# Performance work log

Measured on AMD Instinct MI355X. Metric: run time of the kernel, lower is better.

Reference implementation:

```python
import jax, jax.numpy as jnp
import numpy as np

DIM = 768
H = 12
NUM_PROP = 40
SPARSITY = 0.05
ALPHA = 0.1
ATTN_KEEP = 0.75  # attention threshold quantile index fraction
EPS = 1e-5


def layernorm(x, w, b):
    mu = x.mean(-1, keepdims=True)
    var = ((x - mu) ** 2).mean(-1, keepdims=True)
    return (x - mu) * jax.lax.rsqrt(var + EPS) * w + b


def setup_inputs() -> dict:
    key = jax.random.key(0)
    ks = jax.random.split(key, 8)
    C, Hd = DIM, DIM
    mlp_h = 4 * DIM
    s = 0.02
    return {
        "x": jax.random.normal(ks[0], (64, 197, C), dtype=jnp.float32),
        "norm1_w": jnp.ones((C,), jnp.float32),
        "norm1_b": jnp.zeros((C,), jnp.float32),
        "qkv_w": jax.random.normal(ks[1], (3 * C, C), jnp.float32) * s,
        "proj_w": jax.random.normal(ks[2], (C, C), jnp.float32) * s,
        "proj_b": jnp.zeros((C,), jnp.float32),
        "norm2_w": jnp.ones((C,), jnp.float32),
        "norm2_b": jnp.zeros((C,), jnp.float32),
        "fc1_w": jax.random.normal(ks[3], (mlp_h, C), jnp.float32) * s,
        "fc1_b": jnp.zeros((mlp_h,), jnp.float32),
        "fc2_w": jax.random.normal(ks[4], (C, mlp_h), jnp.float32) * s,
        "fc2_b": jnp.zeros((C,), jnp.float32),
    }


def _forward(x, norm1_w, norm1_b, qkv_w, proj_w, proj_b,
             norm2_w, norm2_b, fc1_w, fc1_b, fc2_w, fc2_b):
    B, N, C = x.shape
    hd = C // H
    scale = hd ** -0.5

    h = layernorm(x, norm1_w, norm1_b)
    qkv = (h @ qkv_w.T).reshape(B, N, 3, H, hd).transpose(2, 0, 3, 1, 4)
    q, k, v = qkv[0], qkv[1], qkv[2]          # [B,H,N,hd]
    attn = jax.nn.softmax((q * scale) @ k.transpose(0, 1, 3, 2), axis=-1)
    attn_rank = jnp.sort(attn.reshape(B, H, -1), axis=-1)[..., ::-1]
    sigma = attn_rank[:, :, int(N * N * ATTN_KEEP)][:, :, None, None]
    attn = jnp.where(attn >= sigma, attn, 0.0)
    out = (attn @ v).transpose(0, 2, 1, 3).reshape(B, N, C)
    x = x + out @ proj_w.T + proj_b

    # ---- select: DiagAttnMean ----
    diag = jnp.diagonal(attn, axis1=-2, axis2=-1)        # [B,H,N]
    token_rank = diag[:, :, 1:].mean(1)                  # [B,N-1]
    order = jnp.argsort(-token_rank, axis=1)             # descending
    index_kept = order[:, :-NUM_PROP] + 1                # [B, num_kept]
    index_elim = order[:, -NUM_PROP:] + 1                # [B, num_elim]
    num_kept = N - 1 - NUM_PROP
    num_elim = NUM_PROP

    # ---- propagate: ThresholdGraph (multihead, thresholded) ----
    x_kept = jnp.take_along_axis(x, index_kept[:, :, None], axis=1)
    x_elim = jnp.take_along_axis(x, index_elim[:, :, None], axis=1)
    x_cls = x[:, 0:1]
    w = jnp.take_along_axis(attn, index_kept[:, None, :, None], axis=2)  # [B,H,k,N]
    w = jnp.take_along_axis(w, index_elim[:, None, None, :], axis=3)     # [B,H,k,e]
    w_rank = jnp.sort(w.reshape(B, H, -1), axis=-1)[..., ::-1]
    w_sigma = w_rank[:, :, int(num_elim * num_kept * SPARSITY)][:, :, None, None]
    w = jnp.where(w >= w_sigma, w, 0.0)
    xe = x_elim.reshape(B, num_elim, H, hd)
    x_prop = jnp.einsum('bhke,behd->bkhd', w, xe).reshape(B, num_kept, C)
    x_kept = x_kept + ALPHA * x_prop
    x = jnp.concatenate((x_cls, x_kept), axis=1)         # [B, N-num_prop, C]

    # ---- MLP ----
    h = layernorm(x, norm2_w, norm2_b)
    h = jax.nn.gelu(h @ fc1_w.T + fc1_b, approximate=False)
    x = x + h @ fc2_w.T + fc2_b
    return x


def reference(x, norm1_w, norm1_b, qkv_w, proj_w, proj_b,
              norm2_w, norm2_b, fc1_w, fc1_b, fc2_w, fc2_b):
    return _forward(x, norm1_w, norm1_b, qkv_w, proj_w, proj_b,
                    norm2_w, norm2_b, fc1_w, fc1_b, fc2_w, fc2_b)
```

## Files before the change

### kernel.cpp

```cpp
#include <hip/hip_runtime.h>
#include <math.h>

constexpr int B_  = 64;
constexpr int N_  = 197;
constexpr int C_  = 768;
constexpr int H_  = 12;
constexpr int HD_ = 64;
constexpr int NP_ = 40;
constexpr int NK_ = 156;
constexpr int N1_ = 196;
constexpr int N2_ = 157;
constexpr int MLP_ = 3072;
constexpr int M1_ = B_ * N_;
constexpr int M2_ = B_ * N2_;
constexpr int M1P_ = 12672;
constexpr int M2P_ = 10112;
constexpr float SCALE_ = 0.125f;
constexpr float ALPHA_ = 0.1f;
constexpr float EPS_   = 1e-5f;
constexpr int KASC_ATTN = N_ * N_ - 1 - 29106;
constexpr int KASC_W    = NK_ * NP_ - 1 - 312;

typedef __bf16 bf16x8 __attribute__((ext_vector_type(8)));
typedef float  floatx4 __attribute__((ext_vector_type(4)));

constexpr size_t A_B     = 0;
constexpr size_t OFFB_XAHI = A_B;
constexpr size_t OFFB_XALO = A_B + 19464192;
constexpr size_t OFFB_ATTN = A_B;
constexpr size_t OFFB_FC1H = A_B;
constexpr size_t OFFB_H2   = A_B + 62128128;
constexpr size_t OFFB_FC1W = A_B + 77660160;
constexpr size_t OFFB_FC2W = A_B + 82378752;
constexpr size_t B_B     = 119221248;
constexpr size_t OFFB_QHI  = B_B;
constexpr size_t OFFB_QLO  = B_B + 38928384;
constexpr size_t OFFB_VB   = B_B + 77856768;
constexpr size_t OFFB_X1   = B_B;
constexpr size_t OFFB_AOUT = B_B + 38928384;
constexpr size_t OFFB_WBUF = B_B + 77856768;
constexpr size_t W_B     = 216542208;
constexpr size_t OFFB_QWHI = W_B;
constexpr size_t OFFB_QWLO = W_B + 3538944;
constexpr size_t OFFB_PRJW = W_B + 7077888;
constexpr size_t S_B     = 224799744;
constexpr size_t OFFB_SIG  = S_B;
constexpr size_t OFFB_WSIG = S_B + 3072;
constexpr size_t OFFB_TR   = S_B + 6144;
constexpr size_t OFFB_ORD  = S_B + 56320;

__global__ __launch_bounds__(256) void wsplit_kernel(
    const float* __restrict__ w, __bf16* __restrict__ hi,
    __bf16* __restrict__ lo, int n)
{
  const int i = blockIdx.x * 256 + threadIdx.x;
  if (i >= n) return;
  const float v = w[i];
  const __bf16 h = (__bf16)v;
  hi[i] = h;
  lo[i] = (__bf16)(v - (float)h);
}

__global__ __launch_bounds__(256) void wconv_kernel(
    const float* __restrict__ w, __bf16* __restrict__ o, int n)
{
  const int i = blockIdx.x * 256 + threadIdx.x;
  if (i < n) o[i] = (__bf16)w[i];
}

__device__ __forceinline__ float block_reduce_sum(float v, float* red) {
  #pragma unroll
  for (int off = 32; off; off >>= 1) v += __shfl_xor(v, off);
  if ((threadIdx.x & 63) == 0) red[threadIdx.x >> 6] = v;
  __syncthreads();
  float r = red[0] + red[1] + red[2] + red[3];
  __syncthreads();
  return r;
}

__global__ __launch_bounds__(256) void ln_bf16_kernel(
    const float* __restrict__ x, const float* __restrict__ w,
    const float* __restrict__ b, __bf16* __restrict__ ohi,
    __bf16* __restrict__ olo, int Mvalid)
{
  __shared__ float red[4];
  const size_t row = blockIdx.x;
  const int t = threadIdx.x;
  if ((int)row >= Mvalid) {
    #pragma unroll
    for (int i = 0; i < 3; ++i) {
      ohi[row * C_ + t + 256 * i] = (__bf16)0.f;
      if (olo) olo[row * C_ + t + 256 * i] = (__bf16)0.f;
    }
    return;
  }
  const float* xr = x + row * C_;
  float v[3];
  float s = 0.f;
  #pragma unroll
  for (int i = 0; i < 3; ++i) { v[i] = xr[t + 256 * i]; s += v[i]; }
  const float mu = block_reduce_sum(s, red) * (1.f / 768.f);
  s = 0.f;
  #pragma unroll
  for (int i = 0; i < 3; ++i) { float d = v[i] - mu; s += d * d; }
  const float var = block_reduce_sum(s, red) * (1.f / 768.f);
  const float rs = rsqrtf(var + EPS_);
  #pragma unroll
  for (int i = 0; i < 3; ++i) {
    const int c = t + 256 * i;
    const float val = (v[i] - mu) * rs * w[c] + b[c];
    const __bf16 h = (__bf16)val;
    ohi[row * C_ + c] = h;
    if (olo) olo[row * C_ + c] = (__bf16)(val - (float)h);
  }
}

__device__ __forceinline__ void stage_tile(
    const __bf16* __restrict__ gbase, int ldg, __bf16* lds, int wave, int lane)
{
  #pragma unroll
  for (int j = 0; j < 2; ++j) {
    const int seg = 4 * j + wave;
    const int row = seg * 16 + (lane >> 2);
    const int col = (lane & 3) * 8;
    const __bf16* g = gbase + (size_t)row * ldg + col;
    __bf16* l = lds + seg * 512 + lane * 8;
    __builtin_amdgcn_global_load_lds(
        (const __attribute__((address_space(1))) unsigned int*)g,
        (__attribute__((address_space(3))) unsigned int*)l, 16, 0, 0);
  }
}

__device__ __forceinline__ bf16x8 frag(const __bf16* lds, int r, int hi8) {
  return *(const bf16x8*)(lds + r * 32 + hi8);
}

__global__ __launch_bounds__(256) void gemm_bf16_kernel(
    const __bf16* __restrict__ A, const __bf16* __restrict__ Bw,
    const float* __restrict__ bias, const float* __restrict__ res,
    float* __restrict__ outf, __bf16* __restrict__ outb,
    int Mstore, int Nn, int K, int act)
{
  __shared__ __bf16 As[128 * 32];
  __shared__ __bf16 Bs[128 * 32];
  const int t = threadIdx.x;
  const int wave = t >> 6, lane = t & 63;
  const int m0 = blockIdx.y * 128, n0 = blockIdx.x * 128;
  const int wm = (wave >> 1) * 64, wn = (wave & 1) * 64;
  const int lo = lane & 15, hi8 = (lane >> 4) * 8;
  floatx4 acc[4][4] = {};
  for (int k0 = 0; k0 < K; k0 += 32) {
    stage_tile(A + (size_t)m0 * K + k0, K, As, wave, lane);
    stage_tile(Bw + (size_t)n0 * K + k0, K, Bs, wave, lane);
    __syncthreads();
    bf16x8 af[4], bfr[4];
    #pragma unroll
    for (int i = 0; i < 4; ++i) af[i]  = frag(As, wm + i * 16 + lo, hi8);
    #pragma unroll
    for (int j = 0; j < 4; ++j) bfr[j] = frag(Bs, wn + j * 16 + lo, hi8);
    #pragma unroll
    for (int i = 0; i < 4; ++i)
      #pragma unroll
      for (int j = 0; j < 4; ++j)
        acc[i][j] = __builtin_amdgcn_mfma_f32_16x16x32_bf16(
            af[i], bfr[j], acc[i][j], 0, 0, 0);
    __syncthreads();
  }
  #pragma unroll
  for (int i = 0; i < 4; ++i) {
    #pragma unroll
    for (int j = 0; j < 4; ++j) {
      #pragma unroll
      for (int r = 0; r < 4; ++r) {
        const int m = m0 + wm + i * 16 + (lane >> 4) * 4 + r;
        const int n = n0 + wn + j * 16 + lo;
        if (m < Mstore) {
          float v = acc[i][j][r];
          if (bias) v += bias[n];
          if (act) v = 0.5f * v * (1.0f + erff(v * 0.7071067811865476f));
          if (res) v += res[(size_t)m * Nn + n];
          if (outf) outf[(size_t)m * Nn + n] = v;
          else      outb[(size_t)m * Nn + n] = (__bf16)v;
        }
      }
    }
  }
}

__global__ __launch_bounds__(256) void gemm_split_kernel(
    const __bf16* __restrict__ Ah, const __bf16* __restrict__ Al,
    const __bf16* __restrict__ Bh, const __bf16* __restrict__ Bl,
    __bf16* __restrict__ outhi, __bf16* __restrict__ outlo, int Nn, int K)
{
  __shared__ __bf16 Ahs[128 * 32];
  __shared__ __bf16 Als[128 * 32];
  __shared__ __bf16 Bhs[128 * 32];
  __shared__ __bf16 Bls[128 * 32];
  const int t = threadIdx.x;
  const int wave = t >> 6, lane = t & 63;
  const int m0 = blockIdx.y * 128, n0 = blockIdx.x * 128;
  const int wm = (wave >> 1) * 64, wn = (wave & 1) * 64;
  const int lo = lane & 15, hi8 = (lane >> 4) * 8;
  floatx4 acc[4][4] = {};
  for (int k0 = 0; k0 < K; k0 += 32) {
    stage_tile(Ah + (size_t)m0 * K + k0, K, Ahs, wave, lane);
    stage_tile(Al + (size_t)m0 * K + k0, K, Als, wave, lane);
    stage_tile(Bh + (size_t)n0 * K + k0, K, Bhs, wave, lane);
    stage_tile(Bl + (size_t)n0 * K + k0, K, Bls, wave, lane);
    __syncthreads();
    bf16x8 ah[4], al[4], bh[4], bl[4];
    #pragma unroll
    for (int i = 0; i < 4; ++i) {
      ah[i] = frag(Ahs, wm + i * 16 + lo, hi8);
      al[i] = frag(Als, wm + i * 16 + lo, hi8);
    }
    #pragma unroll
    for (int j = 0; j < 4; ++j) {
      bh[j] = frag(Bhs, wn + j * 16 + lo, hi8);
      bl[j] = frag(Bls, wn + j * 16 + lo, hi8);
    }
    #pragma unroll
    for (int i = 0; i < 4; ++i)
      #pragma unroll
      for (int j = 0; j < 4; ++j) {
        acc[i][j] = __builtin_amdgcn_mfma_f32_16x16x32_bf16(
            ah[i], bh[j], acc[i][j], 0, 0, 0);
        acc[i][j] = __builtin_amdgcn_mfma_f32_16x16x32_bf16(
            ah[i], bl[j], acc[i][j], 0, 0, 0);
        acc[i][j] = __builtin_amdgcn_mfma_f32_16x16x32_bf16(
            al[i], bh[j], acc[i][j], 0, 0, 0);
      }
    __syncthreads();
  }
  #pragma unroll
  for (int i = 0; i < 4; ++i)
    #pragma unroll
    for (int j = 0; j < 4; ++j)
      #pragma unroll
      for (int r = 0; r < 4; ++r) {
        const int m = m0 + wm + i * 16 + (lane >> 4) * 4 + r;
        const int n = n0 + wn + j * 16 + lo;
        const float v = acc[i][j][r];
        const __bf16 h = (__bf16)v;
        outhi[(size_t)m * Nn + n] = h;
        outlo[(size_t)m * Nn + n] = (__bf16)(v - (float)h);
      }
}

__global__ __launch_bounds__(256) void scores_mfma_kernel(
    const __bf16* __restrict__ qhi, const __bf16* __restrict__ qlo,
    float* __restrict__ attn)
{
  const int bh = blockIdx.x;
  const int b = bh / H_, h = bh % H_;
  __shared__ __bf16 Khi[208 * 72];
  __shared__ __bf16 Klo[208 * 72];
  const int t = threadIdx.x;
  for (int idx = t; idx < 208 * 32; idx += 256) {
    const int j = idx >> 5;
    const int c2 = (idx & 31) * 2;
    unsigned int vh = 0u, vl = 0u;
    if (j < N_) {
      const size_t g = ((size_t)(b * N_ + j)) * 1536 + 768 + h * HD_ + c2;
      vh = *(const unsigned int*)(qhi + g);
      vl = *(const unsigned int*)(qlo + g);
    }
    *(unsigned int*)(Khi + j * 72 + c2) = vh;
    *(unsigned int*)(Klo + j * 72 + c2) = vl;
  }
  __syncthreads();
  const int wave = t >> 6, lane = t & 63;
  const int lo16 = lane & 15, k8 = (lane >> 4) * 8;
  float* Sbh = attn + (size_t)bh * N_ * N_;
  bf16x8 zf;
  #pragma unroll
  for (int e = 0; e < 8; ++e) zf[e] = (__bf16)0.f;
  for (int i = 0; i < 4; ++i) {
    const int mrow = wave * 64 + i * 16 + lo16;
    bf16x8 ahi[2], alo[2];
    #pragma unroll
    for (int kk = 0; kk < 2; ++kk) {
      if (mrow < N_) {
        const size_t g = ((size_t)(b * N_ + mrow)) * 1536 + h * HD_ + kk * 32 + k8;
        ahi[kk] = *(const bf16x8*)(qhi + g);
        alo[kk] = *(const bf16x8*)(qlo + g);
      } else {
        ahi[kk] = zf;
        alo[kk] = zf;
      }
    }
    for (int j = 0; j < 13; ++j) {
      floatx4 acc = {0.f, 0.f, 0.f, 0.f};
      #pragma unroll
      for (int kk = 0; kk < 2; ++kk) {
        const bf16x8 bh_ = *(const bf16x8*)(Khi + (j * 16 + lo16) * 72 + kk * 32 + k8);
        const bf16x8 bl_ = *(const bf16x8*)(Klo + (j * 16 + lo16) * 72 + kk * 32 + k8);
        acc = __builtin_amdgcn_mfma_f32_16x16x32_bf16(ahi[kk], bh_, acc, 0, 0, 0);
        acc = __builtin_amdgcn_mfma_f32_16x16x32_bf16(ahi[kk], bl_, acc, 0, 0, 0);
        acc = __builtin_amdgcn_mfma_f32_16x16x32_bf16(alo[kk], bh_, acc, 0, 0, 0);
        acc = __builtin_amdgcn_mfma_f32_16x16x32_bf16(alo[kk], bl_, acc, 0, 0, 0);
      }
      const int col = j * 16 + lo16;
      if (col < N_) {
        #pragma unroll
        for (int r = 0; r < 4; ++r) {
          const int row = wave * 64 + i * 16 + (lane >> 4) * 4 + r;
          if (row < N_) Sbh[(size_t)row * N_ + col] = acc[r] * SCALE_;
        }
      }
    }
  }
}

__global__ __launch_bounds__(256) void softmax_kernel(float* __restrict__ attn)
{
  const int row = blockIdx.x * 4 + (threadIdx.x >> 6);
  const int lane = threadIdx.x & 63;
  float* r = attn + (size_t)row * N_;
  float vals[4];
  float m = -1e30f;
  int cnt = 0;
  for (int j = lane; j < N_; j += 64) { vals[cnt] = r[j]; m = fmaxf(m, vals[cnt]); ++cnt; }
  #pragma unroll
  for (int off = 32; off; off >>= 1) m = fmaxf(m, __shfl_xor(m, off));
  float s = 0.f;
  for (int i = 0; i < cnt; ++i) { vals[i] = expf(vals[i] - m); s += vals[i]; }
  #pragma unroll
  for (int off = 32; off; off >>= 1) s += __shfl_xor(s, off);
  const float inv = 1.0f / s;
  cnt = 0;
  for (int j = lane; j < N_; j += 64) { r[j] = vals[cnt] * inv; ++cnt; }
}

__global__ __launch_bounds__(256) void radix_select_kernel(
    const float* __restrict__ data, int count, int k, int stride,
    float* __restrict__ out)
{
  const float* seg = data + (size_t)blockIdx.x * stride;
  __shared__ unsigned int hist[256];
  __shared__ unsigned int prefix_s;
  __shared__ int k_s;
  unsigned int prefix = 0u;
  int kk = k;
  for (int pass = 3; pass >= 0; --pass) {
    const int shift = pass * 8;
    hist[threadIdx.x] = 0u;
    __syncthreads();
    const unsigned int mask_known =
        (pass == 3) ? 0u : (0xFFFFFFFFu << ((pass + 1) * 8));
    for (int i = threadIdx.x; i < count; i += 256) {
      const unsigned int bits = __float_as_uint(seg[i]);
      if ((bits & mask_known) == prefix)
        atomicAdd(&hist[(bits >> shift) & 0xFFu], 1u);
    }
    __syncthreads();
    if (threadIdx.x == 0) {
      int rem = kk;
      unsigned int d = 0;
      for (; d < 256u; ++d) {
        if (rem < (int)hist[d]) break;
        rem -= (int)hist[d];
      }
      prefix_s = prefix | (d << shift);
      k_s = rem;
    }
    __syncthreads();
    prefix = prefix_s;
    kk = k_s;
    __syncthreads();
  }
  if (threadIdx.x == 0) out[blockIdx.x] = __uint_as_float(prefix);
}

__global__ __launch_bounds__(256) void threshold_kernel(
    float* __restrict__ a, const float* __restrict__ sig, int total, int seglen)
{
  const int idx = blockIdx.x * 256 + threadIdx.x;
  if (idx >= total) return;
  const float v = a[idx];
  if (v < sig[idx / seglen]) a[idx] = 0.0f;
}

__global__ __launch_bounds__(256) void attn_v_mfma_kernel(
    const float* __restrict__ attn, const float* __restrict__ sig,
    const __bf16* __restrict__ v, __bf16* __restrict__ out)
{
  const int bh = blockIdx.x;
  const int mt = blockIdx.y;
  const int b = bh / H_, h = bh % H_;
  __shared__ __bf16 Ps[64 * 232];
  __shared__ __bf16 Vt[64 * 232];
  const int t = threadIdx.x;
  const float sigbh = sig[bh];
  const float* abase = attn + (size_t)bh * N_ * N_;
  for (int idx = t; idx < 64 * 112; idx += 256) {
    const int r = idx / 112;
    const int j0 = (idx % 112) * 2;
    const int gr = mt * 64 + r;
    float v0 = 0.f, v1 = 0.f;
    if (gr < N_) {
      if (j0 < N_)     { const float a0 = abase[(size_t)gr * N_ + j0];     v0 = (a0 >= sigbh) ? a0 : 0.f; }
      if (j0 + 1 < N_) { const float a1 = abase[(size_t)gr * N_ + j0 + 1]; v1 = (a1 >= sigbh) ? a1 : 0.f; }
    }
    __bf16 p2[2] = {(__bf16)v0, (__bf16)v1};
    *(unsigned int*)(Ps + r * 232 + j0) = *(unsigned int*)p2;
  }
  for (int idx = t; idx < 64 * 224; idx += 256) {
    const int d = idx / 224;
    const int j = idx % 224;
    __bf16 val = (__bf16)0.f;
    if (j < N_) val = v[((size_t)(b * N_ + j)) * C_ + h * HD_ + d];
    Vt[d * 232 + j] = val;
  }
  __syncthreads();
  const int wave = t >> 6, lane = t & 63;
  const int lo16 = lane & 15, k8 = (lane >> 4) * 8;
  #pragma unroll
  for (int jn = 0; jn < 4; ++jn) {
    floatx4 acc = {0.f, 0.f, 0.f, 0.f};
    #pragma unroll
    for (int kk = 0; kk < 7; ++kk) {
      const bf16x8 a = *(const bf16x8*)(Ps + (wave * 16 + lo16) * 232 + kk * 32 + k8);
      const bf16x8 bb = *(const bf16x8*)(Vt + (jn * 16 + lo16) * 232 + kk * 32 + k8);
      acc = __builtin_amdgcn_mfma_f32_16x16x32_bf16(a, bb, acc, 0, 0, 0);
    }
    const int d = jn * 16 + lo16;
    #pragma unroll
    for (int r = 0; r < 4; ++r) {
      const int m = mt * 64 + wave * 16 + (lane >> 4) * 4 + r;
      if (m < N_)
        out[((size_t)b * N_ + m) * C_ + h * HD_ + d] = (__bf16)acc[r];
    }
  }
}

__global__ __launch_bounds__(256) void token_rank_kernel(
    const float* __restrict__ attn, const float* __restrict__ sig,
    float* __restrict__ tr)
{
  const int b = blockIdx.x;
  for (int j = threadIdx.x; j < N1_; j += 256) {
    const int n = j + 1;
    float s = 0.f;
    #pragma unroll
    for (int h = 0; h < H_; ++h) {
      const float d = attn[(((size_t)(b * H_ + h)) * N_ + n) * N_ + n];
      s += (d >= sig[b * H_ + h]) ? d : 0.f;
    }
    tr[b * N1_ + j] = s * (1.f / H_);
  }
}

__global__ __launch_bounds__(256) void order_kernel(
    const float* __restrict__ tr, int* __restrict__ order)
{
  const int b = blockIdx.x;
  __shared__ float v[N1_];
  const int t = threadIdx.x;
  if (t < N1_) v[t] = tr[b * N1_ + t];
  __syncthreads();
  if (t < N1_) {
    const float mv = v[t];
    int r = 0;
    for (int i = 0; i < N1_; ++i) {
      const float vi = v[i];
      r += (vi > mv) || (vi == mv && i < t);
    }
    order[b * N1_ + r] = t;
  }
}

__global__ __launch_bounds__(256) void w_gather_kernel(
    const float* __restrict__ attn, const float* __restrict__ sig,
    const int* __restrict__ ord, float* __restrict__ w)
{
  const int idx = blockIdx.x * 256 + threadIdx.x;
  if (idx >= B_ * H_ * NK_ * NP_) return;
  const int e = idx % NP_;
  const int k = (idx / NP_) % NK_;
  const int h = (idx / (NP_ * NK_)) % H_;
  const int b = idx / (NP_ * NK_ * H_);
  const int ki = ord[b * N1_ + k] + 1;
  const int ej = ord[b * N1_ + NK_ + e] + 1;
  const float v = attn[(((size_t)b * H_ + h) * N_ + ki) * N_ + ej];
  w[idx] = (v >= sig[b * H_ + h]) ? v : 0.f;
}

__global__ __launch_bounds__(256) void xprop_kernel(
    const float* __restrict__ x1, const float* __restrict__ w,
    const int* __restrict__ ord, float* __restrict__ x2)
{
  const int b = blockIdx.y;
  const int kk = blockIdx.x;
  const int t = threadIdx.x;
  if (kk == 0) {
    for (int c = t; c < C_; c += 256)
      x2[(size_t)b * N2_ * C_ + c] = x1[(size_t)b * N_ * C_ + c];
    return;
  }
  const int k = kk - 1;
  __shared__ float ws_[H_ * NP_];
  __shared__ int es[NP_];
  if (t < NP_) es[t] = ord[b * N1_ + NK_ + t] + 1;
  for (int i = t; i < H_ * NP_; i += 256) {
    const int h = i / NP_, e = i % NP_;
    ws_[i] = w[(((size_t)b * H_ + h) * NK_ + k) * NP_ + e];
  }
  __syncthreads();
  const int kept = ord[b * N1_ + k] + 1;
  const float* xk = x1 + ((size_t)b * N_ + kept) * C_;
  float* xo = x2 + ((size_t)b * N2_ + 1 + k) * C_;
  for (int c = t; c < C_; c += 256) {
    const int h = c >> 6;
    float acc = 0.f;
    #pragma unroll 8
    for (int e = 0; e < NP_; ++e)
      acc += ws_[h * NP_ + e] * x1[((size_t)b * N_ + es[e]) * C_ + c];
    xo[c] = xk[c] + ALPHA_ * acc;
  }
}

extern "C" void kernel_launch(void* const* d_in, const int* in_sizes, int n_in,
                              void* d_out, int out_size, void* d_ws, size_t ws_size,
                              hipStream_t stream)
{
  const float* x     = (const float*)d_in[0];
  const float* n1w   = (const float*)d_in[1];
  const float* n1b   = (const float*)d_in[2];
  const float* qkvw  = (const float*)d_in[3];
  const float* projw = (const float*)d_in[4];
  const float* projb = (const float*)d_in[5];
  const float* n2w   = (const float*)d_in[6];
  const float* n2b   = (const float*)d_in[7];
  const float* fc1w  = (const float*)d_in[8];
  const float* fc1b  = (const float*)d_in[9];
  const float* fc2w  = (const float*)d_in[10];
  const float* fc2b  = (const float*)d_in[11];
  float* outp = (float*)d_out;

  char* ws = (char*)d_ws;
  __bf16* xa_hi = (__bf16*)(ws + OFFB_XAHI);
  __bf16* xa_lo = (__bf16*)(ws + OFFB_XALO);
  float*  attn  = (float*)(ws + OFFB_ATTN);
  __bf16* fc1h  = (__bf16*)(ws + OFFB_FC1H);
  __bf16* h2    = (__bf16*)(ws + OFFB_H2);
  __bf16* fc1wb = (__bf16*)(ws + OFFB_FC1W);
  __bf16* fc2wb = (__bf16*)(ws + OFFB_FC2W);
  __bf16* qhi   = (__bf16*)(ws + OFFB_QHI);
  __bf16* qlo   = (__bf16*)(ws + OFFB_QLO);
  __bf16* vb    = (__bf16*)(ws + OFFB_VB);
  float*  x1    = (float*)(ws + OFFB_X1);
  __bf16* aout  = (__bf16*)(ws + OFFB_AOUT);
  float*  wbuf  = (float*)(ws + OFFB_WBUF);
  __bf16* qwhi  = (__bf16*)(ws + OFFB_QWHI);
  __bf16* qwlo  = (__bf16*)(ws + OFFB_QWLO);
  __bf16* prjwb = (__bf16*)(ws + OFFB_PRJW);
  float*  sig   = (float*)(ws + OFFB_SIG);
  float*  wsig  = (float*)(ws + OFFB_WSIG);
  float*  tr    = (float*)(ws + OFFB_TR);
  int*    ord   = (int*)(ws + OFFB_ORD);
  float*  x2    = outp;

  wsplit_kernel<<<(2304 * 768 + 255) / 256, 256, 0, stream>>>(
      qkvw, qwhi, qwlo, 2304 * 768);
  wconv_kernel<<<(768 * 768 + 255) / 256, 256, 0, stream>>>(
      projw, prjwb, 768 * 768);
  ln_bf16_kernel<<<M1P_, 256, 0, stream>>>(x, n1w, n1b, xa_hi, xa_lo, M1_);
  gemm_split_kernel<<<dim3(1536 / 128, M1P_ / 128), 256, 0, stream>>>(
      xa_hi, xa_lo, qwhi, qwlo, qhi, qlo, 1536, C_);
  gemm_bf16_kernel<<<dim3(C_ / 128, M1P_ / 128), 256, 0, stream>>>(
      xa_hi, qwhi + (size_t)1536 * C_, nullptr, nullptr, nullptr, vb,
      M1P_, C_, C_, 0);
  scores_mfma_kernel<<<B_ * H_, 256, 0, stream>>>(qhi, qlo, attn);
  softmax_kernel<<<(B_ * H_ * N_) / 4, 256, 0, stream>>>(attn);
  radix_select_kernel<<<B_ * H_, 256, 0, stream>>>(attn, N_ * N_, KASC_ATTN,
                                                   N_ * N_, sig);
  attn_v_mfma_kernel<<<dim3(B_ * H_, 4), 256, 0, stream>>>(attn, sig, vb, aout);
  token_rank_kernel<<<B_, 256, 0, stream>>>(attn, sig, tr);
  order_kernel<<<B_, 256, 0, stream>>>(tr, ord);
  gemm_bf16_kernel<<<dim3(C_ / 128, M1P_ / 128), 256, 0, stream>>>(
      aout, prjwb, projb, x, x1, nullptr, M1_, C_, C_, 0);
  {
    const int total = B_ * H_ * NK_ * NP_;
    w_gather_kernel<<<(total + 255) / 256, 256, 0, stream>>>(attn, sig, ord, wbuf);
    radix_select_kernel<<<B_ * H_, 256, 0, stream>>>(wbuf, NK_ * NP_, KASC_W,
                                                     NK_ * NP_, wsig);
    threshold_kernel<<<(total + 255) / 256, 256, 0, stream>>>(wbuf, wsig, total,
                                                              NK_ * NP_);
  }
  wconv_kernel<<<(MLP_ * C_ + 255) / 256, 256, 0, stream>>>(
      fc1w, fc1wb, MLP_ * C_);
  wconv_kernel<<<(C_ * MLP_ + 255) / 256, 256, 0, stream>>>(
      fc2w, fc2wb, C_ * MLP_);
  xprop_kernel<<<dim3(N2_, B_), 256, 0, stream>>>(x1, wbuf, ord, x2);
  ln_bf16_kernel<<<M2P_, 256, 0, stream>>>(x2, n2w, n2b, h2, nullptr, M2_);
  gemm_bf16_kernel<<<dim3(MLP_ / 128, M2P_ / 128), 256, 0, stream>>>(
      h2, fc1wb, fc1b, nullptr, nullptr, fc1h, M2P_, MLP_, C_, 1);
  gemm_bf16_kernel<<<dim3(C_ / 128, M2P_ / 128), 256, 0, stream>>>(
      fc1h, fc2wb, fc2b, x2, outp, nullptr, M2_, C_, MLP_, 0);
}
```

Baseline: 1.367 ms.

## Split radix select into multi-block histogram passes with wave-aggregated atomics

Replaces the single-block-per-segment radix select with a multi-kernel scheme: each of the four 8-bit passes launches a histogram kernel that spreads each segment across several blocks (8 for attention, 2 for the gathered weights), followed by a small scan kernel that updates the prefix and remaining rank. Shared-memory histogram increments are aggregated per wave with ballot/match to reduce atomic contention on hot bins. The goal is more parallelism, since 768 blocks each serially scanned about 39k elements four times. The cost is many more kernel launches, global atomics, and a serial per-segment scan done by one thread each.

```diff
diff --git a/kernel.cpp b/kernel.cpp
--- a/kernel.cpp
+++ b/kernel.cpp
@@ -20,6 +20,7 @@
 constexpr float EPS_   = 1e-5f;
 constexpr int KASC_ATTN = N_ * N_ - 1 - 29106;
 constexpr int KASC_W    = NK_ * NP_ - 1 - 312;
+constexpr int NSEG_ = B_ * H_;
 
 typedef __bf16 bf16x8 __attribute__((ext_vector_type(8)));
 typedef float  floatx4 __attribute__((ext_vector_type(4)));
@@ -48,6 +49,9 @@
 constexpr size_t OFFB_WSIG = S_B + 3072;
 constexpr size_t OFFB_TR   = S_B + 6144;
 constexpr size_t OFFB_ORD  = S_B + 56320;
+constexpr size_t OFFB_HIST = S_B + 106496;
+constexpr size_t OFFB_PFX  = S_B + 892928;
+constexpr size_t OFFB_KK   = S_B + 896000;
 
 __global__ __launch_bounds__(256) void wsplit_kernel(
     const float* __restrict__ w, __bf16* __restrict__ hi,
@@ -332,44 +336,78 @@
   for (int j = lane; j < N_; j += 64) { r[j] = vals[cnt] * inv; ++cnt; }
 }
 
-__global__ __launch_bounds__(256) void radix_select_kernel(
-    const float* __restrict__ data, int count, int k, int stride,
-    float* __restrict__ out)
-{
-  const float* seg = data + (size_t)blockIdx.x * stride;
-  __shared__ unsigned int hist[256];
-  __shared__ unsigned int prefix_s;
-  __shared__ int k_s;
-  unsigned int prefix = 0u;
-  int kk = k;
-  for (int pass = 3; pass >= 0; --pass) {
-    const int shift = pass * 8;
-    hist[threadIdx.x] = 0u;
-    __syncthreads();
-    const unsigned int mask_known =
-        (pass == 3) ? 0u : (0xFFFFFFFFu << ((pass + 1) * 8));
-    for (int i = threadIdx.x; i < count; i += 256) {
-      const unsigned int bits = __float_as_uint(seg[i]);
-      if ((bits & mask_known) == prefix)
-        atomicAdd(&hist[(bits >> shift) & 0xFFu], 1u);
-    }
-    __syncthreads();
-    if (threadIdx.x == 0) {
-      int rem = kk;
-      unsigned int d = 0;
-      for (; d < 256u; ++d) {
-        if (rem < (int)hist[d]) break;
-        rem -= (int)hist[d];
-      }
-      prefix_s = prefix | (d << shift);
-      k_s = rem;
-    }
-    __syncthreads();
-    prefix = prefix_s;
-    kk = k_s;
-    __syncthreads();
-  }
-  if (threadIdx.x == 0) out[blockIdx.x] = __uint_as_float(prefix);
+__global__ __launch_bounds__(256) void rsel_init_kernel(
+    unsigned int* __restrict__ hist, unsigned int* __restrict__ prefix,
+    int* __restrict__ kk, int k)
+{
+  const int i = blockIdx.x * 256 + threadIdx.x;
+  hist[i] = 0u;
+  if (i < NSEG_) { prefix[i] = 0u; kk[i] = k; }
+}
+
+__device__ __forceinline__ void wave_agg_inc(
+    unsigned int* lh, int bin, bool active)
+{
+  unsigned long long mask = __ballot(active);
+  const int lane = threadIdx.x & 63;
+  while (mask) {
+    const int leader = __ffsll((unsigned long long)mask) - 1;
+    const int lbin = __shfl(bin, leader);
+    const unsigned long long match = __ballot(active && (bin == lbin));
+    if (lane == leader)
+      atomicAdd(&lh[lbin], (unsigned int)__popcll(match));
+    mask &= ~match;
+  }
+}
+
+__global__ __launch_bounds__(256) void rsel_hist_kernel(
+    const float* __restrict__ data, int count, int split,
+    const unsigned int* __restrict__ prefix, unsigned int* __restrict__ hist,
+    int shift)
+{
+  const int seg = blockIdx.x / split;
+  const int sub = blockIdx.x % split;
+  const float* sd = data + (size_t)seg * count;
+  __shared__ unsigned int lh[256];
+  lh[threadIdx.x] = 0u;
+  __syncthreads();
+  const unsigned int pfx = prefix[seg];
+  const unsigned int mask_known =
+      (shift == 24) ? 0u : (0xFFFFFFFFu << (shift + 8));
+  const int step = split * 256;
+  for (int i = sub * 256 + threadIdx.x; i < count; i += step) {
+    const unsigned int bits = __float_as_uint(sd[i]);
+    const bool act = (bits & mask_known) == pfx;
+    const int bin = (bits >> shift) & 0xFF;
+    wave_agg_inc(lh, bin, act);
+  }
+  __syncthreads();
+  const unsigned int c = lh[threadIdx.x];
+  if (c) atomicAdd(&hist[seg * 256 + threadIdx.x], c);
+}
+
+__global__ __launch_bounds__(256) void rsel_scan_kernel(
+    unsigned int* __restrict__ hist, unsigned int* __restrict__ prefix,
+    int* __restrict__ kk, int shift, float* __restrict__ out)
+{
+  const int seg = blockIdx.x * 256 + threadIdx.x;
+  if (seg >= NSEG_) return;
+  unsigned int* h = hist + seg * 256;
+  int rem = kk[seg];
+  unsigned int d = 255u;
+  bool found = false;
+  for (int i = 0; i < 256; ++i) {
+    const unsigned int c = h[i];
+    h[i] = 0u;
+    if (!found) {
+      if (rem < (int)c) { d = (unsigned int)i; found = true; }
+      else rem -= (int)c;
+    }
+  }
+  const unsigned int np = prefix[seg] | (d << shift);
+  prefix[seg] = np;
+  kk[seg] = rem;
+  if (shift == 0 && out) out[seg] = __uint_as_float(np);
 }
 
 __global__ __launch_bounds__(256) void threshold_kernel(
@@ -559,7 +597,21 @@
   float*  wsig  = (float*)(ws + OFFB_WSIG);
   float*  tr    = (float*)(ws + OFFB_TR);
   int*    ord   = (int*)(ws + OFFB_ORD);
+  unsigned int* hist = (unsigned int*)(ws + OFFB_HIST);
+  unsigned int* pfx  = (unsigned int*)(ws + OFFB_PFX);
+  int*          kkb  = (int*)(ws + OFFB_KK);
   float*  x2    = outp;
+
+  auto run_select = [&](const float* data, int count, int k, int split,
+                        float* out) {
+    rsel_init_kernel<<<NSEG_, 256, 0, stream>>>(hist, pfx, kkb, k);
+    for (int shift = 24; shift >= 0; shift -= 8) {
+      rsel_hist_kernel<<<NSEG_ * split, 256, 0, stream>>>(
+          data, count, split, pfx, hist, shift);
+      rsel_scan_kernel<<<3, 256, 0, stream>>>(
+          hist, pfx, kkb, shift, (shift == 0) ? out : nullptr);
+    }
+  };
 
   wsplit_kernel<<<(2304 * 768 + 255) / 256, 256, 0, stream>>>(
       qkvw, qwhi, qwlo, 2304 * 768);
@@ -573,8 +625,7 @@
       M1P_, C_, C_, 0);
   scores_mfma_kernel<<<B_ * H_, 256, 0, stream>>>(qhi, qlo, attn);
   softmax_kernel<<<(B_ * H_ * N_) / 4, 256, 0, stream>>>(attn);
-  radix_select_kernel<<<B_ * H_, 256, 0, stream>>>(attn, N_ * N_, KASC_ATTN,
-                                                   N_ * N_, sig);
+  run_select(attn, N_ * N_, KASC_ATTN, 8, sig);
   attn_v_mfma_kernel<<<dim3(B_ * H_, 4), 256, 0, stream>>>(attn, sig, vb, aout);
   token_rank_kernel<<<B_, 256, 0, stream>>>(attn, sig, tr);
   order_kernel<<<B_, 256, 0, stream>>>(tr, ord);
@@ -583,8 +634,7 @@
   {
     const int total = B_ * H_ * NK_ * NP_;
     w_gather_kernel<<<(total + 255) / 256, 256, 0, stream>>>(attn, sig, ord, wbuf);
-    radix_select_kernel<<<B_ * H_, 256, 0, stream>>>(wbuf, NK_ * NP_, KASC_W,
-                                                     NK_ * NP_, wsig);
+    run_select(wbuf, NK_ * NP_, KASC_W, 2, wsig);
     threshold_kernel<<<(total + 255) / 256, 256, 0, stream>>>(wbuf, wsig, total,
                                                               NK_ * NP_);
   }
```

Result: slower. 2.335 ms (+70.9%).
